# Kernel optimization log

Hardware: AMD Instinct MI355X
Metric: run time of the kernel (lower is better)

Reference implementation:

```python
import jax, jax.numpy as jnp
import numpy as np

E, T, H, I = 8, 1024, 2048, 1408

def setup_inputs() -> dict:
    key = jax.random.key(0)
    k1, k2, k3, k4 = jax.random.split(key, 4)
    scale = 1.0 / np.sqrt(H)
    return {
        "x": jax.random.normal(k1, (E, T, H), dtype=jnp.float32),
        "gate_proj": jax.random.normal(k2, (E, H, I), dtype=jnp.float32) * scale,
        "up_proj": jax.random.normal(k3, (E, H, I), dtype=jnp.float32) * scale,
        "down_proj": jax.random.normal(k4, (E, I, H), dtype=jnp.float32) * (1.0 / np.sqrt(I)),
    }

def reference(x, gate_proj, up_proj, down_proj):
    # x: [E, T, H]; per-expert SwiGLU MLP via batched matmuls
    gate = jax.nn.silu(jnp.einsum('eth,ehi->eti', x, gate_proj))
    up = jnp.einsum('eth,ehi->eti', x, up_proj)
    return jnp.einsum('eti,eih->eth', gate * up, down_proj)
```

## Files before the change

kernel.cpp:

```cpp
#include <hip/hip_runtime.h>
#include <hip/hip_bf16.h>
#include <stdint.h>

#define NE 8
#define NT 1024
#define NH 2048
#define NI 1408
#define NI2 (2 * NI)

typedef __attribute__((ext_vector_type(8))) short          bf16x8;
typedef __attribute__((ext_vector_type(8))) unsigned short u16x8;
typedef __attribute__((ext_vector_type(4))) unsigned short u16x4;
typedef __attribute__((ext_vector_type(4))) float          f32x4;

__device__ __forceinline__ unsigned short f2bf(float f) {
  union { float f; uint32_t u; } v; v.f = f;
  uint32_t u = v.u;
  return (unsigned short)((u + 0x7FFFu + ((u >> 16) & 1u)) >> 16);
}

__device__ __forceinline__ void gload_lds16(const void* g, void* l) {
  __builtin_amdgcn_global_load_lds(
      (const __attribute__((address_space(1))) uint32_t*)g,
      (__attribute__((address_space(3))) uint32_t*)l, 16, 0, 0);
}

#define WAITV(n) asm volatile("s_waitcnt vmcnt(" #n ")" ::: "memory")
#define BAR() do { __builtin_amdgcn_sched_barrier(0); \
                   __builtin_amdgcn_s_barrier();      \
                   __builtin_amdgcn_sched_barrier(0); } while (0)

__global__ __launch_bounds__(256) void cvt_bf16(const float* __restrict__ src,
                                                unsigned short* __restrict__ dst,
                                                int n8) {
  int i = blockIdx.x * blockDim.x + threadIdx.x;
  const int stride = gridDim.x * blockDim.x;
  for (; i < n8; i += stride) {
    const float4 f0 = ((const float4*)src)[i * 2];
    const float4 f1 = ((const float4*)src)[i * 2 + 1];
    u16x8 o;
    o[0] = f2bf(f0.x); o[1] = f2bf(f0.y); o[2] = f2bf(f0.z); o[3] = f2bf(f0.w);
    o[4] = f2bf(f1.x); o[5] = f2bf(f1.y); o[6] = f2bf(f1.z); o[7] = f2bf(f1.w);
    ((u16x8*)dst)[i] = o;
  }
}

__global__ __launch_bounds__(256) void transpose_cvt(
    const float* __restrict__ src, unsigned short* __restrict__ dst,
    int R, int C, long estride, int ilv, int radd) {
  __shared__ float tile[64][65];
  const int e  = blockIdx.z;
  const int c0 = blockIdx.x * 64;
  const int r0 = blockIdx.y * 64;
  const float* s = src + (size_t)e * R * C;
  unsigned short* d = dst + (size_t)e * estride;
  const int tid = threadIdx.x;
  const int tr  = tid >> 4;
  const int tc  = (tid & 15) * 4;
  #pragma unroll
  for (int it = 0; it < 4; ++it) {
    const int r = it * 16 + tr;
    float4 v = *(const float4*)(s + (size_t)(r0 + r) * C + c0 + tc);
    tile[r][tc + 0] = v.x; tile[r][tc + 1] = v.y;
    tile[r][tc + 2] = v.z; tile[r][tc + 3] = v.w;
  }
  __syncthreads();
  #pragma unroll
  for (int it = 0; it < 4; ++it) {
    const int oc = it * 16 + tr;
    const int c  = c0 + oc;
    const int ro = ilv ? ((((c >> 4) << 5) | (c & 15)) | radd) : c;
    u16x4 o;
    o[0] = f2bf(tile[tc + 0][oc]);
    o[1] = f2bf(tile[tc + 1][oc]);
    o[2] = f2bf(tile[tc + 2][oc]);
    o[3] = f2bf(tile[tc + 3][oc]);
    *(u16x4*)(d + (size_t)ro * R + r0 + tc) = o;
  }
}

template <int NBY, int KDIM, int MODE>
__global__ __launch_bounds__(512, 2) void gemm_pipe(
    const unsigned short* __restrict__ Ag,
    const unsigned short* __restrict__ Bg,
    void* __restrict__ outp) {
  constexpr int KSTEPS = KDIM / 64;
  constexpr int NBLK   = NE * NBY * 8;
  constexpr int CHUNK  = NBLK / 8;

  __shared__ __align__(16) unsigned short As[3][128 * 64];
  __shared__ __align__(16) unsigned short Bs[3][256 * 64];

  const int flat = blockIdx.x;
  const int orig = (flat & 7) * CHUNK + (flat >> 3);
  const int bx   = orig & 7;
  const int rest = orig >> 3;
  const int by   = rest % NBY;
  const int e    = rest / NBY;

  const int bm  = bx * 128;
  const int bnn = by * 256;

  const int tid  = threadIdx.x;
  const int lane = tid & 63;
  const int w    = tid >> 6;
  const int wrm  = (w >> 2) * 64;
  const int wcn  = (w & 3) * 64;

  const unsigned short* Ae = Ag + (size_t)e * 1024 * KDIM;
  const unsigned short* Be = Bg + (size_t)e * (NBY * 256) * KDIM;

  const int l8 = lane >> 3;
  const int jx = (lane & 7) ^ l8;
  const unsigned short* aAg = Ae + (size_t)(bm  + w * 16 + l8) * KDIM + jx * 8;
  const unsigned short* aBg = Be + (size_t)(bnn + w * 32 + l8) * KDIM + jx * 8;

  f32x4 acc[4][4];
  #pragma unroll
  for (int i = 0; i < 4; ++i)
    #pragma unroll
    for (int j = 0; j < 4; ++j) acc[i][j] = f32x4{0.f, 0.f, 0.f, 0.f};

  const int aoff = (lane & 15) * 128 + ((((lane >> 4) << 4)) ^ ((lane & 7) << 4));

  auto STAGE = [&](unsigned short* Ad, unsigned short* Bd, int kstep) {
    const int kb = kstep * 64;
    #pragma unroll
    for (int q = 0; q < 2; ++q)
      gload_lds16(aAg + (size_t)q * 8 * KDIM + kb, Ad + (w * 16 + q * 8) * 64);
    #pragma unroll
    for (int q = 0; q < 4; ++q)
      gload_lds16(aBg + (size_t)q * 8 * KDIM + kb, Bd + (w * 32 + q * 8) * 64);
  };

  auto COMPUTE = [&](const unsigned short* Ab_, const unsigned short* Bb_) {
    const char* Ab = (const char*)Ab_ + wrm * 128;
    const char* Bb = (const char*)Bb_ + wcn * 128;
    bf16x8 af[4][2], bf[4][2];
    #pragma unroll
    for (int mi = 0; mi < 4; ++mi) {
      af[mi][0] = *(const bf16x8*)(Ab + mi * 2048 + aoff);
      af[mi][1] = *(const bf16x8*)(Ab + mi * 2048 + (aoff ^ 64));
    }
    #pragma unroll
    for (int nj = 0; nj < 4; ++nj) {
      bf[nj][0] = *(const bf16x8*)(Bb + nj * 2048 + aoff);
      bf[nj][1] = *(const bf16x8*)(Bb + nj * 2048 + (aoff ^ 64));
    }
    __builtin_amdgcn_s_setprio(1);
    #pragma unroll
    for (int kk = 0; kk < 2; ++kk)
      #pragma unroll
      for (int mi = 0; mi < 4; ++mi)
        #pragma unroll
        for (int nj = 0; nj < 4; ++nj)
          acc[mi][nj] = __builtin_amdgcn_mfma_f32_16x16x32_bf16(
              af[mi][kk], bf[nj][kk], acc[mi][nj], 0, 0, 0);
    __builtin_amdgcn_s_setprio(0);
  };

  unsigned short *a0 = As[0], *a1 = As[1], *a2 = As[2];
  unsigned short *b0 = Bs[0], *b1 = Bs[1], *b2 = Bs[2];

  STAGE(a0, b0, 0);
  STAGE(a1, b1, 1);

  #pragma unroll 1
  for (int s = 0; s < KSTEPS; ++s) {
    if (s + 2 < KSTEPS) {
      STAGE(a2, b2, s + 2);
      WAITV(12);
    } else if (s + 2 == KSTEPS) {
      WAITV(6);
    } else {
      WAITV(0);
    }
    BAR();
    COMPUTE(a0, b0);
    BAR();
    unsigned short* t;
    t = a0; a0 = a1; a1 = a2; a2 = t;
    t = b0; b0 = b1; b1 = b2; b2 = t;
  }

  const int crow = (lane >> 4) * 4;
  const int ccol = lane & 15;
  if constexpr (MODE == 0) {
    float* oe = (float*)outp + (size_t)e * 1024 * (NBY * 256);
    #pragma unroll
    for (int mi = 0; mi < 4; ++mi)
      #pragma unroll
      for (int nj = 0; nj < 4; ++nj)
        #pragma unroll
        for (int j = 0; j < 4; ++j) {
          const int row = bm + wrm + mi * 16 + crow + j;
          const int col = bnn + wcn + nj * 16 + ccol;
          oe[(size_t)row * (NBY * 256) + col] = acc[mi][nj][j];
        }
  } else {
    unsigned short* he = (unsigned short*)outp + (size_t)e * 1024 * (NBY * 128);
    const int hcb = by * 128 + (wcn >> 1);
    #pragma unroll
    for (int mi = 0; mi < 4; ++mi)
      #pragma unroll
      for (int p = 0; p < 2; ++p)
        #pragma unroll
        for (int j = 0; j < 4; ++j) {
          const float g = acc[mi][2 * p][j];
          const float u = acc[mi][2 * p + 1][j];
          const float sv = g / (1.0f + __expf(-g)) * u;
          const int row = bm + wrm + mi * 16 + crow + j;
          const int col = hcb + p * 16 + ccol;
          he[(size_t)row * (NBY * 128) + col] = f2bf(sv);
        }
  }
}

extern "C" void kernel_launch(void* const* d_in, const int* in_sizes, int n_in,
                              void* d_out, int out_size, void* d_ws, size_t ws_size,
                              hipStream_t stream) {
  const float* x    = (const float*)d_in[0];
  const float* gate = (const float*)d_in[1];
  const float* up   = (const float*)d_in[2];
  const float* down = (const float*)d_in[3];
  float* out = (float*)d_out;

  unsigned short* x_bf = (unsigned short*)d_ws;
  unsigned short* wcat = x_bf + (size_t)NE * NT * NH;
  unsigned short* dT   = wcat + (size_t)NE * NI2 * NH;
  unsigned short* hb   = dT   + (size_t)NE * NH * NI;

  cvt_bf16<<<2048, 256, 0, stream>>>(x, x_bf, NE * NT * NH / 8);

  transpose_cvt<<<dim3(NI / 64, NH / 64, NE), 256, 0, stream>>>(
      gate, wcat, NH, NI, (long)NI2 * NH, 1, 0);
  transpose_cvt<<<dim3(NI / 64, NH / 64, NE), 256, 0, stream>>>(
      up, wcat, NH, NI, (long)NI2 * NH, 1, 16);
  transpose_cvt<<<dim3(NH / 64, NI / 64, NE), 256, 0, stream>>>(
      down, dT, NI, NH, (long)NH * NI, 0, 0);

  gemm_pipe<11, NH, 1><<<NE * 11 * 8, 512, 0, stream>>>(x_bf, wcat, hb);
  gemm_pipe<8, NI, 0><<<NE * 8 * 8, 512, 0, stream>>>(hb, dT, out);
}
```

Measured before the change: 334.7 us.

## Enlarge GEMM tiles to 256x256 with double-buffered quadrant-interleaved pipeline

Each GEMM block now computes a 256x256 output tile instead of 128x256, so each wave holds a 128x64 accumulator and more MFMA work is done per LDS byte and global load. The 3-stage LDS ring is replaced by a 2-stage double buffer. The next tile's A and B loads are issued between four quadrant MFMA phases separated by barriers. This trades fewer blocks (half the grid) and much higher register pressure, which may cut occupancy, for better data reuse.

Result: faster. 274.8 us (-17.9%).

```diff
diff --git a/kernel.cpp b/kernel.cpp
--- a/kernel.cpp
+++ b/kernel.cpp
@@ -25,7 +25,7 @@
       (__attribute__((address_space(3))) uint32_t*)l, 16, 0, 0);
 }
 
-#define WAITV(n) asm volatile("s_waitcnt vmcnt(" #n ")" ::: "memory")
+#define WAITV0() asm volatile("s_waitcnt vmcnt(0)" ::: "memory")
 #define BAR() do { __builtin_amdgcn_sched_barrier(0); \
                    __builtin_amdgcn_s_barrier();      \
                    __builtin_amdgcn_sched_barrier(0); } while (0)
@@ -84,27 +84,26 @@
     const unsigned short* __restrict__ Ag,
     const unsigned short* __restrict__ Bg,
     void* __restrict__ outp) {
-  constexpr int KSTEPS = KDIM / 64;
-  constexpr int NBLK   = NE * NBY * 8;
-  constexpr int CHUNK  = NBLK / 8;
-
-  __shared__ __align__(16) unsigned short As[3][128 * 64];
-  __shared__ __align__(16) unsigned short Bs[3][256 * 64];
+  constexpr int KT    = KDIM / 64;
+  constexpr int NBLK  = NE * NBY * 4;
+  constexpr int CHUNK = NBLK / 8;
+
+  __shared__ __align__(16) unsigned short As[2][256 * 64];
+  __shared__ __align__(16) unsigned short Bs[2][256 * 64];
 
   const int flat = blockIdx.x;
   const int orig = (flat & 7) * CHUNK + (flat >> 3);
-  const int bx   = orig & 7;
-  const int rest = orig >> 3;
-  const int by   = rest % NBY;
-  const int e    = rest / NBY;
-
-  const int bm  = bx * 128;
+  const int bx   = orig & 3;
+  const int by   = (orig >> 2) % NBY;
+  const int e    = (orig >> 2) / NBY;
+
+  const int bm  = bx * 256;
   const int bnn = by * 256;
 
   const int tid  = threadIdx.x;
   const int lane = tid & 63;
   const int w    = tid >> 6;
-  const int wrm  = (w >> 2) * 64;
+  const int wrm  = (w >> 2) * 128;
   const int wcn  = (w & 3) * 64;
 
   const unsigned short* Ae = Ag + (size_t)e * 1024 * KDIM;
@@ -112,75 +111,121 @@
 
   const int l8 = lane >> 3;
   const int jx = (lane & 7) ^ l8;
-  const unsigned short* aAg = Ae + (size_t)(bm  + w * 16 + l8) * KDIM + jx * 8;
+  const unsigned short* aAg = Ae + (size_t)(bm  + w * 32 + l8) * KDIM + jx * 8;
   const unsigned short* aBg = Be + (size_t)(bnn + w * 32 + l8) * KDIM + jx * 8;
 
-  f32x4 acc[4][4];
+  f32x4 acc[8][4];
   #pragma unroll
-  for (int i = 0; i < 4; ++i)
+  for (int i = 0; i < 8; ++i)
     #pragma unroll
     for (int j = 0; j < 4; ++j) acc[i][j] = f32x4{0.f, 0.f, 0.f, 0.f};
 
   const int aoff = (lane & 15) * 128 + ((((lane >> 4) << 4)) ^ ((lane & 7) << 4));
 
-  auto STAGE = [&](unsigned short* Ad, unsigned short* Bd, int kstep) {
-    const int kb = kstep * 64;
-    #pragma unroll
-    for (int q = 0; q < 2; ++q)
-      gload_lds16(aAg + (size_t)q * 8 * KDIM + kb, Ad + (w * 16 + q * 8) * 64);
+  auto STAGE_A = [&](unsigned short* dst, int t) {
+    const unsigned short* g = aAg + (size_t)t * 64;
     #pragma unroll
     for (int q = 0; q < 4; ++q)
-      gload_lds16(aBg + (size_t)q * 8 * KDIM + kb, Bd + (w * 32 + q * 8) * 64);
+      gload_lds16(g + (size_t)q * 8 * KDIM, dst + (w * 32 + q * 8) * 64);
   };
-
-  auto COMPUTE = [&](const unsigned short* Ab_, const unsigned short* Bb_) {
-    const char* Ab = (const char*)Ab_ + wrm * 128;
-    const char* Bb = (const char*)Bb_ + wcn * 128;
-    bf16x8 af[4][2], bf[4][2];
+  auto STAGE_B = [&](unsigned short* dst, int t) {
+    const unsigned short* g = aBg + (size_t)t * 64;
+    #pragma unroll
+    for (int q = 0; q < 4; ++q)
+      gload_lds16(g + (size_t)q * 8 * KDIM, dst + (w * 32 + q * 8) * 64);
+  };
+
+  unsigned short *Ac = As[0], *Bc = Bs[0], *An = As[1], *Bn = Bs[1];
+
+  STAGE_A(Ac, 0);
+  STAGE_B(Bc, 0);
+  WAITV0();
+  BAR();
+
+  #pragma unroll 1
+  for (int t = 0; t < KT; ++t) {
+    const bool st = (t + 1 < KT);
+    const char* Ab = (const char*)Ac + wrm * 128;
+    const char* Bb = (const char*)Bc + wcn * 128;
+    bf16x8 a0[4][2], a1[4][2], b0[2][2], b1[2][2];
+
     #pragma unroll
     for (int mi = 0; mi < 4; ++mi) {
-      af[mi][0] = *(const bf16x8*)(Ab + mi * 2048 + aoff);
-      af[mi][1] = *(const bf16x8*)(Ab + mi * 2048 + (aoff ^ 64));
-    }
-    #pragma unroll
-    for (int nj = 0; nj < 4; ++nj) {
-      bf[nj][0] = *(const bf16x8*)(Bb + nj * 2048 + aoff);
-      bf[nj][1] = *(const bf16x8*)(Bb + nj * 2048 + (aoff ^ 64));
-    }
-    __builtin_amdgcn_s_setprio(1);
-    #pragma unroll
-    for (int kk = 0; kk < 2; ++kk)
-      #pragma unroll
-      for (int mi = 0; mi < 4; ++mi)
-        #pragma unroll
-        for (int nj = 0; nj < 4; ++nj)
+      a0[mi][0] = *(const bf16x8*)(Ab + mi * 2048 + aoff);
+      a0[mi][1] = *(const bf16x8*)(Ab + mi * 2048 + (aoff ^ 64));
+    }
+    #pragma unroll
+    for (int nj = 0; nj < 2; ++nj) {
+      b0[nj][0] = *(const bf16x8*)(Bb + nj * 2048 + aoff);
+      b0[nj][1] = *(const bf16x8*)(Bb + nj * 2048 + (aoff ^ 64));
+    }
+    if (st) STAGE_A(An, t + 1);
+    BAR();
+    __builtin_amdgcn_s_setprio(1);
+    #pragma unroll
+    for (int kk = 0; kk < 2; ++kk)
+      #pragma unroll
+      for (int mi = 0; mi < 4; ++mi)
+        #pragma unroll
+        for (int nj = 0; nj < 2; ++nj)
           acc[mi][nj] = __builtin_amdgcn_mfma_f32_16x16x32_bf16(
-              af[mi][kk], bf[nj][kk], acc[mi][nj], 0, 0, 0);
-    __builtin_amdgcn_s_setprio(0);
-  };
-
-  unsigned short *a0 = As[0], *a1 = As[1], *a2 = As[2];
-  unsigned short *b0 = Bs[0], *b1 = Bs[1], *b2 = Bs[2];
-
-  STAGE(a0, b0, 0);
-  STAGE(a1, b1, 1);
-
-  #pragma unroll 1
-  for (int s = 0; s < KSTEPS; ++s) {
-    if (s + 2 < KSTEPS) {
-      STAGE(a2, b2, s + 2);
-      WAITV(12);
-    } else if (s + 2 == KSTEPS) {
-      WAITV(6);
-    } else {
-      WAITV(0);
-    }
-    BAR();
-    COMPUTE(a0, b0);
-    BAR();
-    unsigned short* t;
-    t = a0; a0 = a1; a1 = a2; a2 = t;
-    t = b0; b0 = b1; b1 = b2; b2 = t;
+              a0[mi][kk], b0[nj][kk], acc[mi][nj], 0, 0, 0);
+    __builtin_amdgcn_s_setprio(0);
+    BAR();
+
+    #pragma unroll
+    for (int nj = 0; nj < 2; ++nj) {
+      b1[nj][0] = *(const bf16x8*)(Bb + (2 + nj) * 2048 + aoff);
+      b1[nj][1] = *(const bf16x8*)(Bb + (2 + nj) * 2048 + (aoff ^ 64));
+    }
+    if (st) STAGE_B(Bn, t + 1);
+    BAR();
+    __builtin_amdgcn_s_setprio(1);
+    #pragma unroll
+    for (int kk = 0; kk < 2; ++kk)
+      #pragma unroll
+      for (int mi = 0; mi < 4; ++mi)
+        #pragma unroll
+        for (int nj = 0; nj < 2; ++nj)
+          acc[mi][2 + nj] = __builtin_amdgcn_mfma_f32_16x16x32_bf16(
+              a0[mi][kk], b1[nj][kk], acc[mi][2 + nj], 0, 0, 0);
+    __builtin_amdgcn_s_setprio(0);
+    BAR();
+
+    #pragma unroll
+    for (int mi = 0; mi < 4; ++mi) {
+      a1[mi][0] = *(const bf16x8*)(Ab + 8192 + mi * 2048 + aoff);
+      a1[mi][1] = *(const bf16x8*)(Ab + 8192 + mi * 2048 + (aoff ^ 64));
+    }
+    BAR();
+    __builtin_amdgcn_s_setprio(1);
+    #pragma unroll
+    for (int kk = 0; kk < 2; ++kk)
+      #pragma unroll
+      for (int mi = 0; mi < 4; ++mi)
+        #pragma unroll
+        for (int nj = 0; nj < 2; ++nj)
+          acc[4 + mi][2 + nj] = __builtin_amdgcn_mfma_f32_16x16x32_bf16(
+              a1[mi][kk], b1[nj][kk], acc[4 + mi][2 + nj], 0, 0, 0);
+    __builtin_amdgcn_s_setprio(0);
+    BAR();
+
+    __builtin_amdgcn_s_setprio(1);
+    #pragma unroll
+    for (int kk = 0; kk < 2; ++kk)
+      #pragma unroll
+      for (int mi = 0; mi < 4; ++mi)
+        #pragma unroll
+        for (int nj = 0; nj < 2; ++nj)
+          acc[4 + mi][nj] = __builtin_amdgcn_mfma_f32_16x16x32_bf16(
+              a1[mi][kk], b0[nj][kk], acc[4 + mi][nj], 0, 0, 0);
+    __builtin_amdgcn_s_setprio(0);
+    if (st) WAITV0();
+    BAR();
+
+    unsigned short* tp;
+    tp = Ac; Ac = An; An = tp;
+    tp = Bc; Bc = Bn; Bn = tp;
   }
 
   const int crow = (lane >> 4) * 4;
@@ -188,7 +233,7 @@
   if constexpr (MODE == 0) {
     float* oe = (float*)outp + (size_t)e * 1024 * (NBY * 256);
     #pragma unroll
-    for (int mi = 0; mi < 4; ++mi)
+    for (int mi = 0; mi < 8; ++mi)
       #pragma unroll
       for (int nj = 0; nj < 4; ++nj)
         #pragma unroll
@@ -201,7 +246,7 @@
     unsigned short* he = (unsigned short*)outp + (size_t)e * 1024 * (NBY * 128);
     const int hcb = by * 128 + (wcn >> 1);
     #pragma unroll
-    for (int mi = 0; mi < 4; ++mi)
+    for (int mi = 0; mi < 8; ++mi)
       #pragma unroll
       for (int p = 0; p < 2; ++p)
         #pragma unroll
@@ -239,6 +284,6 @@
   transpose_cvt<<<dim3(NH / 64, NI / 64, NE), 256, 0, stream>>>(
       down, dT, NI, NH, (long)NH * NI, 0, 0);
 
-  gemm_pipe<11, NH, 1><<<NE * 11 * 8, 512, 0, stream>>>(x_bf, wcat, hb);
-  gemm_pipe<8, NI, 0><<<NE * 8 * 8, 512, 0, stream>>>(hb, dT, out);
-}
+  gemm_pipe<11, NH, 1><<<NE * 11 * 4, 512, 0, stream>>>(x_bf, wcat, hb);
+  gemm_pipe<8, NI, 0><<<NE * 8 * 4, 512, 0, stream>>>(hb, dT, out);
+}
```

## Split each K-step into two half-phases interleaving LDS reads, prefetch and MFMA

Applied to the files above, without the earlier changes.

Restructures the GEMM main loop so each 64-wide K tile is processed in two 32-wide halves, with the fragment loads for each half issued just before its MFMA block. The global-to-LDS prefetch for tile t+2 is issued after the first half's fragments are read, and the vmcnt wait is moved to the second half. The aim is to shrink register pressure and overlap LDS fragment loads and global prefetch with MFMA work across waves. In exchange it adds barriers per iteration (four instead of two), which can add synchronisation stalls.

Result: faster. 276.8 us (-17.3%).

```diff
diff --git a/kernel.cpp b/kernel.cpp
--- a/kernel.cpp
+++ b/kernel.cpp
@@ -84,9 +84,8 @@
     const unsigned short* __restrict__ Ag,
     const unsigned short* __restrict__ Bg,
     void* __restrict__ outp) {
-  constexpr int KSTEPS = KDIM / 64;
-  constexpr int NBLK   = NE * NBY * 8;
-  constexpr int CHUNK  = NBLK / 8;
+  constexpr int KT    = KDIM / 64;
+  constexpr int CHUNK = NBY * 8;
 
   __shared__ __align__(16) unsigned short As[3][128 * 64];
   __shared__ __align__(16) unsigned short Bs[3][256 * 64];
@@ -123,8 +122,8 @@
 
   const int aoff = (lane & 15) * 128 + ((((lane >> 4) << 4)) ^ ((lane & 7) << 4));
 
-  auto STAGE = [&](unsigned short* Ad, unsigned short* Bd, int kstep) {
-    const int kb = kstep * 64;
+  auto STAGE = [&](unsigned short* Ad, unsigned short* Bd, int t) {
+    const int kb = t * 64;
     #pragma unroll
     for (int q = 0; q < 2; ++q)
       gload_lds16(aAg + (size_t)q * 8 * KDIM + kb, Ad + (w * 16 + q * 8) * 64);
@@ -133,54 +132,57 @@
       gload_lds16(aBg + (size_t)q * 8 * KDIM + kb, Bd + (w * 32 + q * 8) * 64);
   };
 
-  auto COMPUTE = [&](const unsigned short* Ab_, const unsigned short* Bb_) {
-    const char* Ab = (const char*)Ab_ + wrm * 128;
-    const char* Bb = (const char*)Bb_ + wcn * 128;
-    bf16x8 af[4][2], bf[4][2];
-    #pragma unroll
-    for (int mi = 0; mi < 4; ++mi) {
-      af[mi][0] = *(const bf16x8*)(Ab + mi * 2048 + aoff);
-      af[mi][1] = *(const bf16x8*)(Ab + mi * 2048 + (aoff ^ 64));
-    }
-    #pragma unroll
-    for (int nj = 0; nj < 4; ++nj) {
-      bf[nj][0] = *(const bf16x8*)(Bb + nj * 2048 + aoff);
-      bf[nj][1] = *(const bf16x8*)(Bb + nj * 2048 + (aoff ^ 64));
-    }
+  unsigned short *A0 = As[0], *A1 = As[1], *A2 = As[2];
+  unsigned short *B0 = Bs[0], *B1 = Bs[1], *B2 = Bs[2];
+
+  STAGE(A0, B0, 0);
+  STAGE(A1, B1, 1);
+  WAITV(6);
+  BAR();
+
+  #pragma unroll 1
+  for (int t = 0; t < KT; ++t) {
+    const char* Ab = (const char*)A0 + wrm * 128;
+    const char* Bb = (const char*)B0 + wcn * 128;
+    const bool st = (t + 2 < KT);
+
+    bf16x8 aa[4], bb[4];
+    #pragma unroll
+    for (int mi = 0; mi < 4; ++mi) aa[mi] = *(const bf16x8*)(Ab + mi * 2048 + aoff);
+    #pragma unroll
+    for (int nj = 0; nj < 4; ++nj) bb[nj] = *(const bf16x8*)(Bb + nj * 2048 + aoff);
+    if (st) STAGE(A2, B2, t + 2);
+    BAR();
     __builtin_amdgcn_s_setprio(1);
     #pragma unroll
-    for (int kk = 0; kk < 2; ++kk)
-      #pragma unroll
-      for (int mi = 0; mi < 4; ++mi)
-        #pragma unroll
-        for (int nj = 0; nj < 4; ++nj)
-          acc[mi][nj] = __builtin_amdgcn_mfma_f32_16x16x32_bf16(
-              af[mi][kk], bf[nj][kk], acc[mi][nj], 0, 0, 0);
+    for (int mi = 0; mi < 4; ++mi)
+      #pragma unroll
+      for (int nj = 0; nj < 4; ++nj)
+        acc[mi][nj] = __builtin_amdgcn_mfma_f32_16x16x32_bf16(
+            aa[mi], bb[nj], acc[mi][nj], 0, 0, 0);
     __builtin_amdgcn_s_setprio(0);
-  };
-
-  unsigned short *a0 = As[0], *a1 = As[1], *a2 = As[2];
-  unsigned short *b0 = Bs[0], *b1 = Bs[1], *b2 = Bs[2];
-
-  STAGE(a0, b0, 0);
-  STAGE(a1, b1, 1);
-
-  #pragma unroll 1
-  for (int s = 0; s < KSTEPS; ++s) {
-    if (s + 2 < KSTEPS) {
-      STAGE(a2, b2, s + 2);
-      WAITV(12);
-    } else if (s + 2 == KSTEPS) {
-      WAITV(6);
-    } else {
-      WAITV(0);
-    }
-    BAR();
-    COMPUTE(a0, b0);
-    BAR();
-    unsigned short* t;
-    t = a0; a0 = a1; a1 = a2; a2 = t;
-    t = b0; b0 = b1; b1 = b2; b2 = t;
+    BAR();
+
+    bf16x8 a2[4], b2[4];
+    #pragma unroll
+    for (int mi = 0; mi < 4; ++mi) a2[mi] = *(const bf16x8*)(Ab + mi * 2048 + (aoff ^ 64));
+    #pragma unroll
+    for (int nj = 0; nj < 4; ++nj) b2[nj] = *(const bf16x8*)(Bb + nj * 2048 + (aoff ^ 64));
+    if (st) { WAITV(6); } else { WAITV(0); }
+    BAR();
+    __builtin_amdgcn_s_setprio(1);
+    #pragma unroll
+    for (int mi = 0; mi < 4; ++mi)
+      #pragma unroll
+      for (int nj = 0; nj < 4; ++nj)
+        acc[mi][nj] = __builtin_amdgcn_mfma_f32_16x16x32_bf16(
+            a2[mi], b2[nj], acc[mi][nj], 0, 0, 0);
+    __builtin_amdgcn_s_setprio(0);
+    BAR();
+
+    unsigned short* tp;
+    tp = A0; A0 = A1; A1 = A2; A2 = tp;
+    tp = B0; B0 = B1; B1 = B2; B2 = tp;
   }
 
   const int crow = (lane >> 4) * 4;
```

## Switch GEMMs to 128x128 tiles with double-buffered async prefetch

Applied to the files above, without the earlier changes.

Replaces the 128x256, 512-thread triple-buffered GEMM with a 128x128, 256-thread kernel using two LDS buffers. The next K-tile is issued after the fragment reads, and each iteration waits with vmcnt(0) and a single barrier. The second barrier and the setprio hints are dropped. This doubles the block count and cuts LDS use to raise occupancy, but the pipeline is shallower and each operand is loaded from global memory more often.

New measurement: 286.9 us. 14.3% less time.

```diff
diff --git a/kernel.cpp b/kernel.cpp
--- a/kernel.cpp
+++ b/kernel.cpp
@@ -25,7 +25,7 @@
       (__attribute__((address_space(3))) uint32_t*)l, 16, 0, 0);
 }
 
-#define WAITV(n) asm volatile("s_waitcnt vmcnt(" #n ")" ::: "memory")
+#define WAITV0() asm volatile("s_waitcnt vmcnt(0)" ::: "memory")
 #define BAR() do { __builtin_amdgcn_sched_barrier(0); \
                    __builtin_amdgcn_s_barrier();      \
                    __builtin_amdgcn_sched_barrier(0); } while (0)
@@ -80,40 +80,39 @@
 }
 
 template <int NBY, int KDIM, int MODE>
-__global__ __launch_bounds__(512, 2) void gemm_pipe(
+__global__ __launch_bounds__(256, 2) void gemm_async(
     const unsigned short* __restrict__ Ag,
     const unsigned short* __restrict__ Bg,
     void* __restrict__ outp) {
-  constexpr int KSTEPS = KDIM / 64;
-  constexpr int NBLK   = NE * NBY * 8;
-  constexpr int CHUNK  = NBLK / 8;
-
-  __shared__ __align__(16) unsigned short As[3][128 * 64];
-  __shared__ __align__(16) unsigned short Bs[3][256 * 64];
+  constexpr int KT    = KDIM / 64;
+  constexpr int CHUNK = NBY * 8;
+
+  __shared__ __align__(16) unsigned short As[2][128 * 64];
+  __shared__ __align__(16) unsigned short Bs[2][128 * 64];
 
   const int flat = blockIdx.x;
   const int orig = (flat & 7) * CHUNK + (flat >> 3);
-  const int bx   = orig & 7;
-  const int rest = orig >> 3;
-  const int by   = rest % NBY;
-  const int e    = rest / NBY;
+  const int e    = orig / CHUNK;
+  const int r    = orig % CHUNK;
+  const int by   = r >> 3;
+  const int bx   = r & 7;
 
   const int bm  = bx * 128;
-  const int bnn = by * 256;
+  const int bnn = by * 128;
 
   const int tid  = threadIdx.x;
   const int lane = tid & 63;
   const int w    = tid >> 6;
-  const int wrm  = (w >> 2) * 64;
-  const int wcn  = (w & 3) * 64;
+  const int wrm  = (w >> 1) * 64;
+  const int wcn  = (w & 1) * 64;
 
   const unsigned short* Ae = Ag + (size_t)e * 1024 * KDIM;
-  const unsigned short* Be = Bg + (size_t)e * (NBY * 256) * KDIM;
+  const unsigned short* Be = Bg + (size_t)e * (NBY * 128) * KDIM;
 
   const int l8 = lane >> 3;
   const int jx = (lane & 7) ^ l8;
-  const unsigned short* aAg = Ae + (size_t)(bm  + w * 16 + l8) * KDIM + jx * 8;
-  const unsigned short* aBg = Be + (size_t)(bnn + w * 32 + l8) * KDIM + jx * 8;
+  const unsigned short* aA = Ae + (size_t)(bm  + w * 32 + l8) * KDIM + jx * 8;
+  const unsigned short* aB = Be + (size_t)(bnn + w * 32 + l8) * KDIM + jx * 8;
 
   f32x4 acc[4][4];
   #pragma unroll
@@ -123,31 +122,34 @@
 
   const int aoff = (lane & 15) * 128 + ((((lane >> 4) << 4)) ^ ((lane & 7) << 4));
 
-  auto STAGE = [&](unsigned short* Ad, unsigned short* Bd, int kstep) {
-    const int kb = kstep * 64;
-    #pragma unroll
-    for (int q = 0; q < 2; ++q)
-      gload_lds16(aAg + (size_t)q * 8 * KDIM + kb, Ad + (w * 16 + q * 8) * 64);
+  auto STAGE = [&](unsigned short* Ad, unsigned short* Bd, int t) {
+    const int kb = t * 64;
     #pragma unroll
     for (int q = 0; q < 4; ++q)
-      gload_lds16(aBg + (size_t)q * 8 * KDIM + kb, Bd + (w * 32 + q * 8) * 64);
+      gload_lds16(aA + (size_t)q * 8 * KDIM + kb, Ad + (w * 32 + q * 8) * 64);
+    #pragma unroll
+    for (int q = 0; q < 4; ++q)
+      gload_lds16(aB + (size_t)q * 8 * KDIM + kb, Bd + (w * 32 + q * 8) * 64);
   };
 
-  auto COMPUTE = [&](const unsigned short* Ab_, const unsigned short* Bb_) {
-    const char* Ab = (const char*)Ab_ + wrm * 128;
-    const char* Bb = (const char*)Bb_ + wcn * 128;
-    bf16x8 af[4][2], bf[4][2];
+  auto ITER = [&](int t, const unsigned short* Ac, const unsigned short* Bc,
+                  unsigned short* An, unsigned short* Bn) {
+    WAITV0();
+    BAR();
+    const char* Ab = (const char*)Ac + wrm * 128;
+    const char* Bb = (const char*)Bc + wcn * 128;
+    bf16x8 a[4][2], b[4][2];
     #pragma unroll
     for (int mi = 0; mi < 4; ++mi) {
-      af[mi][0] = *(const bf16x8*)(Ab + mi * 2048 + aoff);
-      af[mi][1] = *(const bf16x8*)(Ab + mi * 2048 + (aoff ^ 64));
+      a[mi][0] = *(const bf16x8*)(Ab + mi * 2048 + aoff);
+      a[mi][1] = *(const bf16x8*)(Ab + mi * 2048 + (aoff ^ 64));
     }
     #pragma unroll
     for (int nj = 0; nj < 4; ++nj) {
-      bf[nj][0] = *(const bf16x8*)(Bb + nj * 2048 + aoff);
-      bf[nj][1] = *(const bf16x8*)(Bb + nj * 2048 + (aoff ^ 64));
+      b[nj][0] = *(const bf16x8*)(Bb + nj * 2048 + aoff);
+      b[nj][1] = *(const bf16x8*)(Bb + nj * 2048 + (aoff ^ 64));
     }
-    __builtin_amdgcn_s_setprio(1);
+    if (t + 1 < KT) STAGE(An, Bn, t + 1);
     #pragma unroll
     for (int kk = 0; kk < 2; ++kk)
       #pragma unroll
@@ -155,38 +157,21 @@
         #pragma unroll
         for (int nj = 0; nj < 4; ++nj)
           acc[mi][nj] = __builtin_amdgcn_mfma_f32_16x16x32_bf16(
-              af[mi][kk], bf[nj][kk], acc[mi][nj], 0, 0, 0);
-    __builtin_amdgcn_s_setprio(0);
+              a[mi][kk], b[nj][kk], acc[mi][nj], 0, 0, 0);
   };
 
-  unsigned short *a0 = As[0], *a1 = As[1], *a2 = As[2];
-  unsigned short *b0 = Bs[0], *b1 = Bs[1], *b2 = Bs[2];
-
-  STAGE(a0, b0, 0);
-  STAGE(a1, b1, 1);
+  STAGE(As[0], Bs[0], 0);
 
   #pragma unroll 1
-  for (int s = 0; s < KSTEPS; ++s) {
-    if (s + 2 < KSTEPS) {
-      STAGE(a2, b2, s + 2);
-      WAITV(12);
-    } else if (s + 2 == KSTEPS) {
-      WAITV(6);
-    } else {
-      WAITV(0);
-    }
-    BAR();
-    COMPUTE(a0, b0);
-    BAR();
-    unsigned short* t;
-    t = a0; a0 = a1; a1 = a2; a2 = t;
-    t = b0; b0 = b1; b1 = b2; b2 = t;
+  for (int t = 0; t < KT; t += 2) {
+    ITER(t,     As[0], Bs[0], As[1], Bs[1]);
+    ITER(t + 1, As[1], Bs[1], As[0], Bs[0]);
   }
 
   const int crow = (lane >> 4) * 4;
   const int ccol = lane & 15;
   if constexpr (MODE == 0) {
-    float* oe = (float*)outp + (size_t)e * 1024 * (NBY * 256);
+    float* oe = (float*)outp + (size_t)e * 1024 * (NBY * 128);
     #pragma unroll
     for (int mi = 0; mi < 4; ++mi)
       #pragma unroll
@@ -195,11 +180,11 @@
         for (int j = 0; j < 4; ++j) {
           const int row = bm + wrm + mi * 16 + crow + j;
           const int col = bnn + wcn + nj * 16 + ccol;
-          oe[(size_t)row * (NBY * 256) + col] = acc[mi][nj][j];
+          oe[(size_t)row * (NBY * 128) + col] = acc[mi][nj][j];
         }
   } else {
-    unsigned short* he = (unsigned short*)outp + (size_t)e * 1024 * (NBY * 128);
-    const int hcb = by * 128 + (wcn >> 1);
+    unsigned short* he = (unsigned short*)outp + (size_t)e * 1024 * (NBY * 64);
+    const int hcb = by * 64 + (wcn >> 1);
     #pragma unroll
     for (int mi = 0; mi < 4; ++mi)
       #pragma unroll
@@ -211,7 +196,7 @@
           const float sv = g / (1.0f + __expf(-g)) * u;
           const int row = bm + wrm + mi * 16 + crow + j;
           const int col = hcb + p * 16 + ccol;
-          he[(size_t)row * (NBY * 128) + col] = f2bf(sv);
+          he[(size_t)row * (NBY * 64) + col] = f2bf(sv);
         }
   }
 }
@@ -239,6 +224,6 @@
   transpose_cvt<<<dim3(NH / 64, NI / 64, NE), 256, 0, stream>>>(
       down, dT, NI, NH, (long)NH * NI, 0, 0);
 
-  gemm_pipe<11, NH, 1><<<NE * 11 * 8, 512, 0, stream>>>(x_bf, wcat, hb);
-  gemm_pipe<8, NI, 0><<<NE * 8 * 8, 512, 0, stream>>>(hb, dT, out);
-}
+  gemm_async<22, NH, 1><<<NE * 22 * 8, 256, 0, stream>>>(x_bf, wcat, hb);
+  gemm_async<16, NI, 0><<<NE * 16 * 8, 256, 0, stream>>>(hb, dT, out);
+}
```
